# Optimization experiments

Hardware: AMD Instinct MI355X
Metric: run time of the kernel (lower is better)

The kernel has to match this reference:

```python
import jax, jax.numpy as jnp
import numpy as np

K = 5          # number of spline bins
B = 5.0        # tail bound
HIDDEN = 8
MIN_W = 1e-3; MIN_H = 1e-3; MIN_D = 1e-3  # RQS defaults (Durkan et al.)


def setup_inputs() -> dict:
    n, d = 32768, 64
    L = d - 1
    P = 3 * K - 1
    ks = jax.random.split(jax.random.key(0), 8)
    x = jax.random.normal(ks[0], (n, d), jnp.float32) * 2.0
    init_param = jax.random.uniform(ks[1], (P,), jnp.float32, -0.5, 0.5)
    # ragged first layers: layer l (predicts dim l+1) sees x[:, :l+1]; zero-pad to width L
    mask = (jnp.arange(L)[None, :] <= jnp.arange(L)[:, None]).astype(jnp.float32)
    W1 = jax.random.normal(ks[2], (L, L, HIDDEN), jnp.float32) * 0.2 * mask[:, :, None]
    b1 = jax.random.normal(ks[3], (L, HIDDEN), jnp.float32) * 0.1
    W2 = jax.random.normal(ks[4], (L, HIDDEN, HIDDEN), jnp.float32) * 0.2
    b2 = jax.random.normal(ks[5], (L, HIDDEN), jnp.float32) * 0.1
    W3 = jax.random.normal(ks[6], (L, HIDDEN, P), jnp.float32) * 0.2
    b3 = jax.random.normal(ks[7], (L, P), jnp.float32) * 0.1
    return {"x": x, "init_param": init_param, "W1": W1, "b1": b1,
            "W2": W2, "b2": b2, "W3": W3, "b3": b3}


def _rqs(xf, Wu, Hu, Du):
    # xf: (M,), Wu/Hu: (M,K), Du: (M,K-1) -- vectorized unconstrained RQS, forward
    inside = (xf >= -B) & (xf <= B)
    const = float(np.log(np.exp(1.0 - MIN_D) - 1.0))
    Dpad = jnp.pad(Du, ((0, 0), (1, 1)), constant_values=const)

    widths = MIN_W + (1.0 - MIN_W * K) * jax.nn.softmax(Wu, axis=-1)
    cumw = jnp.pad(jnp.cumsum(widths, -1), ((0, 0), (1, 0)))
    cumw = 2.0 * B * cumw - B
    cumw = cumw.at[:, 0].set(-B).at[:, -1].set(B)
    widths = cumw[:, 1:] - cumw[:, :-1]

    heights = MIN_H + (1.0 - MIN_H * K) * jax.nn.softmax(Hu, axis=-1)
    cumh = jnp.pad(jnp.cumsum(heights, -1), ((0, 0), (1, 0)))
    cumh = 2.0 * B * cumh - B
    cumh = cumh.at[:, 0].set(-B).at[:, -1].set(B)
    heights = cumh[:, 1:] - cumh[:, :-1]

    derivs = MIN_D + jax.nn.softplus(Dpad)  # (M, K+1)

    xc = jnp.clip(xf, -B, B)
    idx = jnp.clip(jnp.sum(xc[:, None] >= cumw, axis=-1) - 1, 0, K - 1)
    take = lambda a: jnp.take_along_axis(a, idx[:, None], axis=-1)[:, 0]

    icw, ibw = take(cumw), take(widths)
    ich, ih = take(cumh), take(heights)
    idl = take(heights / widths)
    idv = take(derivs)
    idvp1 = take(derivs[:, 1:])

    theta = (xc - icw) / ibw
    tmt = theta * (1.0 - theta)
    num = ih * (idl * theta * theta + idv * tmt)
    den = idl + (idv + idvp1 - 2.0 * idl) * tmt
    out = ich + num / den
    dnum = idl * idl * (idvp1 * theta * theta + 2.0 * idl * tmt + idv * (1.0 - theta) ** 2)
    ld = jnp.log(dnum) - 2.0 * jnp.log(den)
    return jnp.where(inside, out, xf), jnp.where(inside, ld, 0.0)


def reference(x, init_param, W1, b1, W2, b2, W3, b3):
    n, d = x.shape
    L = d - 1
    P = 3 * K - 1
    # mask re-applied so padded W1 entries are exactly inert (ragged Linear(i, hidden))
    mask = (jnp.arange(L)[None, :] <= jnp.arange(L)[:, None]).astype(x.dtype)
    h = jnp.tanh(jnp.einsum('nj,ljh->lnh', x[:, :L], W1 * mask[:, :, None]) + b1[:, None, :])
    h = jnp.tanh(jnp.einsum('lnh,lhg->lng', h, W2) + b2[:, None, :])
    out = jnp.einsum('lng,lgp->lnp', h, W3) + b3[:, None, :]      # (L, n, P)
    p0 = jnp.broadcast_to(init_param, (1, n, P))                  # dim 0 uses init_param
    params = jnp.concatenate([p0, out], axis=0).reshape(d * n, P)  # dim-major, matches Ws layout
    Wu, Hu, Du = params[:, :K], params[:, K:2 * K], params[:, 2 * K:]
    xf = x.T.reshape(-1)  # x.transpose(0,1).flatten()
    zs, lds = _rqs(xf, Wu, Hu, Du)
    # NOTE: faithfully replicates the original's reshape of the dim-major flat
    # vector directly to (n, d) (as in the torch source).
    return zs.reshape(n, d), lds.reshape(n, d).sum(axis=1)
```

## Files before the change

kernel.cpp:

```cpp
#include <hip/hip_runtime.h>
#include <hip/hip_bf16.h>
#include <math.h>

#define KK 5
#define Bc 5.0f
#define NN 32768
#define DD 64
#define LL 63
#define PP 14
#define MIN_Wc 0.001f
#define MIN_Hc 0.001f
#define MIN_Dc 0.001f

typedef float f4 __attribute__((ext_vector_type(4)));
typedef float f32x4 __attribute__((ext_vector_type(4)));
typedef float f2 __attribute__((ext_vector_type(2)));
typedef short short8 __attribute__((ext_vector_type(8)));

__device__ __forceinline__ float rcp_fast(float v)  { return __builtin_amdgcn_rcpf(v); }
__device__ __forceinline__ float exp_fast(float v)  { return __expf(v); }
__device__ __forceinline__ float log_fast(float v)  { return __logf(v); }
__device__ __forceinline__ float tanh_fast(float v) {
    float e = exp_fast(2.0f * v);
    return 1.0f - 2.0f * rcp_fast(e + 1.0f);
}
__device__ __forceinline__ float softplus_fast(float v) {
    return (v > 15.0f) ? v : log_fast(1.0f + exp_fast(v));
}
__device__ __forceinline__ ushort to_bf16u(float v) {
    __hip_bfloat16 b = __float2bfloat16(v);
    return *(ushort*)&b;
}
__device__ __forceinline__ f2 splat2(float v) { f2 r; r.x = v; r.y = v; return r; }

__global__ __launch_bounds__(256) void pack_b1(const float* __restrict__ W1,
                                               ushort* __restrict__ Bp) {
    int id = blockIdx.x * 256 + threadIdx.x;
    int n = id >> 6, k = id & 63;
    float v = 0.f;
    if (n < 504 && k < 63) {
        int l = n >> 3, h = n & 7;
        v = W1[(l * 63 + k) * 8 + h];
    }
    Bp[id] = to_bf16u(v);
}

__device__ __forceinline__ short8 pack_a(f4 v0, f4 v1) {
    short8 a;
    a[0] = (short)to_bf16u(v0.x); a[1] = (short)to_bf16u(v0.y);
    a[2] = (short)to_bf16u(v0.z); a[3] = (short)to_bf16u(v0.w);
    a[4] = (short)to_bf16u(v1.x); a[5] = (short)to_bf16u(v1.y);
    a[6] = (short)to_bf16u(v1.z); a[7] = (short)to_bf16u(v1.w);
    return a;
}

__device__ __forceinline__ void do_dim(
    int dd, float xf, uint4 hv, int s0, int lane, int bx,
    const float* __restrict__ init_param,
    const float* __restrict__ W2, const float* __restrict__ b2,
    const float* __restrict__ W3, const float* __restrict__ b3,
    float* __restrict__ out)
{
    float p[PP];
    if (dd == 0) {
        #pragma unroll
        for (int i = 0; i < PP; ++i) p[i] = init_param[i];
    } else {
        const int l = dd - 1;
        float h1f[8];
        h1f[0] = __uint_as_float(hv.x << 16);
        h1f[1] = __uint_as_float(hv.x & 0xFFFF0000u);
        h1f[2] = __uint_as_float(hv.y << 16);
        h1f[3] = __uint_as_float(hv.y & 0xFFFF0000u);
        h1f[4] = __uint_as_float(hv.z << 16);
        h1f[5] = __uint_as_float(hv.z & 0xFFFF0000u);
        h1f[6] = __uint_as_float(hv.w << 16);
        h1f[7] = __uint_as_float(hv.w & 0xFFFF0000u);

        const f2* w2p = (const f2*)(W2 + l * 64);
        const f2* b2p = (const f2*)(b2 + l * 8);
        f2 h2p0 = b2p[0], h2p1 = b2p[1], h2p2 = b2p[2], h2p3 = b2p[3];
        #pragma unroll
        for (int h = 0; h < 8; ++h) {
            f2 av = splat2(h1f[h]);
            h2p0 += av * w2p[h * 4];
            h2p1 += av * w2p[h * 4 + 1];
            h2p2 += av * w2p[h * 4 + 2];
            h2p3 += av * w2p[h * 4 + 3];
        }
        float h2f[8];
        h2f[0] = tanh_fast(h2p0.x); h2f[1] = tanh_fast(h2p0.y);
        h2f[2] = tanh_fast(h2p1.x); h2f[3] = tanh_fast(h2p1.y);
        h2f[4] = tanh_fast(h2p2.x); h2f[5] = tanh_fast(h2p2.y);
        h2f[6] = tanh_fast(h2p3.x); h2f[7] = tanh_fast(h2p3.y);

        const f2* w3p = (const f2*)(W3 + l * 112);
        const f2* b3p = (const f2*)(b3 + l * PP);
        f2 pp0 = b3p[0], pp1 = b3p[1], pp2 = b3p[2], pp3 = b3p[3];
        f2 pp4 = b3p[4], pp5 = b3p[5], pp6 = b3p[6];
        #pragma unroll
        for (int g = 0; g < 8; ++g) {
            f2 av = splat2(h2f[g]);
            pp0 += av * w3p[g * 7];
            pp1 += av * w3p[g * 7 + 1];
            pp2 += av * w3p[g * 7 + 2];
            pp3 += av * w3p[g * 7 + 3];
            pp4 += av * w3p[g * 7 + 4];
            pp5 += av * w3p[g * 7 + 5];
            pp6 += av * w3p[g * 7 + 6];
        }
        p[0] = pp0.x; p[1] = pp0.y; p[2]  = pp1.x; p[3]  = pp1.y;
        p[4] = pp2.x; p[5] = pp2.y; p[6]  = pp3.x; p[7]  = pp3.y;
        p[8] = pp4.x; p[9] = pp4.y; p[10] = pp5.x; p[11] = pp5.y;
        p[12] = pp6.x; p[13] = pp6.y;
    }

    f2 e0, e1, e2, e3, e4;
    e0.x = exp_fast(p[0]); e0.y = exp_fast(p[KK]);
    e1.x = exp_fast(p[1]); e1.y = exp_fast(p[KK + 1]);
    e2.x = exp_fast(p[2]); e2.y = exp_fast(p[KK + 2]);
    e3.x = exp_fast(p[3]); e3.y = exp_fast(p[KK + 3]);
    e4.x = exp_fast(p[4]); e4.y = exp_fast(p[KK + 4]);
    f2 es = e0 + e1 + e2 + e3 + e4;
    f2 nrm; nrm.x = 0.995f * rcp_fast(es.x); nrm.y = 0.995f * rcp_fast(es.y);

    const f2 minv = {MIN_Wc, MIN_Hc};
    f2 cb0 = splat2(-Bc), acc2 = splat2(0.f);
    acc2 += minv + nrm * e0;  f2 cb1 = splat2(2.f * Bc) * acc2 - splat2(Bc);
    acc2 += minv + nrm * e1;  f2 cb2 = splat2(2.f * Bc) * acc2 - splat2(Bc);
    acc2 += minv + nrm * e2;  f2 cb3 = splat2(2.f * Bc) * acc2 - splat2(Bc);
    acc2 += minv + nrm * e3;  f2 cb4 = splat2(2.f * Bc) * acc2 - splat2(Bc);
    f2 cb5 = splat2(Bc);

    float d0 = 1.0f, d5 = 1.0f;
    float d1 = MIN_Dc + softplus_fast(p[10]);
    float d2 = MIN_Dc + softplus_fast(p[11]);
    float d3 = MIN_Dc + softplus_fast(p[12]);
    float d4 = MIN_Dc + softplus_fast(p[13]);

    const float xc = fminf(fmaxf(xf, -Bc), Bc);

    float icw = cb0.x, ich = cb0.y;
    float ibw = cb1.x - cb0.x, ih = cb1.y - cb0.y;
    float idv = d0, idvp1 = d1;
    {
        bool c = xc >= cb1.x; f2 dif = cb2 - cb1;
        icw = c ? cb1.x : icw; ich = c ? cb1.y : ich;
        ibw = c ? dif.x : ibw; ih  = c ? dif.y : ih;
        idv = c ? d1 : idv; idvp1 = c ? d2 : idvp1;
    }
    {
        bool c = xc >= cb2.x; f2 dif = cb3 - cb2;
        icw = c ? cb2.x : icw; ich = c ? cb2.y : ich;
        ibw = c ? dif.x : ibw; ih  = c ? dif.y : ih;
        idv = c ? d2 : idv; idvp1 = c ? d3 : idvp1;
    }
    {
        bool c = xc >= cb3.x; f2 dif = cb4 - cb3;
        icw = c ? cb3.x : icw; ich = c ? cb3.y : ich;
        ibw = c ? dif.x : ibw; ih  = c ? dif.y : ih;
        idv = c ? d3 : idv; idvp1 = c ? d4 : idvp1;
    }
    {
        bool c = xc >= cb4.x; f2 dif = cb5 - cb4;
        icw = c ? cb4.x : icw; ich = c ? cb4.y : ich;
        ibw = c ? dif.x : ibw; ih  = c ? dif.y : ih;
        idv = c ? d4 : idv; idvp1 = c ? d5 : idvp1;
    }

    const float ibw_r = rcp_fast(ibw);
    const float idl = ih * ibw_r;
    const float theta = (xc - icw) * ibw_r;
    const float omt = 1.0f - theta;
    const float tmt = theta * omt;
    const float num = ih * (idl * theta * theta + idv * tmt);
    const float den = idl + (idv + idvp1 - 2.0f * idl) * tmt;
    const float dr = rcp_fast(den);
    const float outv = ich + num * dr;
    const float dnum = idl * idl * (idvp1 * theta * theta + 2.0f * idl * tmt + idv * omt * omt);
    const float ld = log_fast(dnum * dr * dr);

    const bool inside = (xf >= -Bc) && (xf <= Bc);
    const float z = inside ? outv : xf;
    float ldv = inside ? ld : 0.0f;

    out[dd * NN + s0 + lane] = z;

    #pragma unroll
    for (int off = 32; off > 0; off >>= 1) ldv += __shfl_down(ldv, off);
    if (lane == 0) out[NN * DD + dd * (NN / 64) + bx] = ldv;
}

#define H1S 136
__global__ __launch_bounds__(256, 8) void fused_kernel(
    const float* __restrict__ x, const float* __restrict__ init_param,
    const ushort* __restrict__ Bp, const float* __restrict__ b1,
    const float* __restrict__ W2, const float* __restrict__ b2,
    const float* __restrict__ W3, const float* __restrict__ b3,
    float* __restrict__ out)
{
    __shared__ ushort h1c[64 * H1S];
    const int tid = threadIdx.x;
    const int s0 = blockIdx.x * 64;
    const int y  = blockIdx.y;
    const int bx = blockIdx.x;
    const int lane = tid & 63;
    const int wave = __builtin_amdgcn_readfirstlane(tid >> 6);
    const int ln = lane & 15, qg = lane >> 4;
    const int m0 = wave * 16;

    const float* xrow = x + (size_t)(s0 + lane) * 64;
    const int db = y * 16 + 1 + wave * 4;
    float xv0 = xrow[db];
    float xv1 = xrow[db + 1];
    float xv2 = xrow[db + 2];
    float xv3 = xrow[(y == 3 && wave == 3) ? 0 : db + 3];

    short8 a0, a1;
    {
        const float* xr = x + (size_t)(s0 + m0 + ln) * 64 + qg * 8;
        a0 = pack_a(*(const f4*)xr, *(const f4*)(xr + 4));
        a1 = (y >= 2) ? pack_a(*(const f4*)(xr + 32), *(const f4*)(xr + 36)) : a0;
    }

    #pragma unroll
    for (int nt = 0; nt < 8; ++nt) {
        int ncol = y * 128 + nt * 16 + ln;
        const short8* bp8 = (const short8*)(Bp + ncol * 64 + qg * 8);
        f32x4 acc = {0.f, 0.f, 0.f, 0.f};
        acc = __builtin_amdgcn_mfma_f32_16x16x32_bf16(a0, bp8[0], acc, 0, 0, 0);
        if (y >= 2)
            acc = __builtin_amdgcn_mfma_f32_16x16x32_bf16(a1, bp8[4], acc, 0, 0, 0);
        float bias = (ncol < 504) ? b1[ncol] : 0.f;
        #pragma unroll
        for (int r = 0; r < 4; ++r) {
            float v = tanh_fast(acc[r] + bias);
            h1c[(m0 + qg * 4 + r) * H1S + nt * 16 + ln] = to_bf16u(v);
        }
    }
    __syncthreads();

    const uint4* hp = (const uint4*)&h1c[lane * H1S + wave * 32];
    uint4 hv0 = hp[0], hv1 = hp[1], hv2 = hp[2], hv3 = hp[3];

    const int d0_ = db;
    do_dim(d0_,     xv0, hv0, s0, lane, bx, init_param, W2, b2, W3, b3, out);
    do_dim(d0_ + 1, xv1, hv1, s0, lane, bx, init_param, W2, b2, W3, b3, out);
    do_dim(d0_ + 2, xv2, hv2, s0, lane, bx, init_param, W2, b2, W3, b3, out);
    do_dim((y == 3 && wave == 3) ? 0 : d0_ + 3,
                    xv3, hv3, s0, lane, bx, init_param, W2, b2, W3, b3, out);
}

extern "C" void kernel_launch(void* const* d_in, const int* in_sizes, int n_in,
                              void* d_out, int out_size, void* d_ws, size_t ws_size,
                              hipStream_t stream) {
    const float* x          = (const float*)d_in[0];
    const float* init_param = (const float*)d_in[1];
    const float* W1         = (const float*)d_in[2];
    const float* b1         = (const float*)d_in[3];
    const float* W2         = (const float*)d_in[4];
    const float* b2         = (const float*)d_in[5];
    const float* W3         = (const float*)d_in[6];
    const float* b3         = (const float*)d_in[7];
    float* out = (float*)d_out;

    ushort* Bp = (ushort*)d_ws;

    pack_b1<<<128, 256, 0, stream>>>(W1, Bp);
    fused_kernel<<<dim3(512, 4), 256, 0, stream>>>(x, init_param, Bp, b1,
                                                   W2, b2, W3, b3, out);
}
```

Measured before the change: 112.3 us.

## Stage per-layer MLP weights in padded LDS and defer softplus to selected bin

Each block now copies the W2, b2, W3 and b3 slices for its 16 layers into shared memory, padded to 16-float rows so the per-lane matvecs use aligned 128-bit LDS reads instead of scalar global loads. The RQS derivative softplus is computed only for the two selected knots instead of all four, which cuts transcendental work. The launch-bounds occupancy hint drops from 8 to 5 to make room for the extra shared memory and registers, so fewer waves may be resident to hide latency.

```diff
diff --git a/kernel.cpp b/kernel.cpp
--- a/kernel.cpp
+++ b/kernel.cpp
@@ -32,6 +32,7 @@
     return *(ushort*)&b;
 }
 __device__ __forceinline__ f2 splat2(float v) { f2 r; r.x = v; r.y = v; return r; }
+__device__ __forceinline__ f4 splat4(float v) { f4 r; r.x = v; r.y = v; r.z = v; r.w = v; return r; }
 
 __global__ __launch_bounds__(256) void pack_b1(const float* __restrict__ W1,
                                                ushort* __restrict__ Bp) {
@@ -54,19 +55,20 @@
     return a;
 }
 
+#define WSL 216
+
 __device__ __forceinline__ void do_dim(
-    int dd, float xf, uint4 hv, int s0, int lane, int bx,
-    const float* __restrict__ init_param,
-    const float* __restrict__ W2, const float* __restrict__ b2,
-    const float* __restrict__ W3, const float* __restrict__ b3,
-    float* __restrict__ out)
+    int dd, const float* wp, float xf, uint4 hv, int s0, int lane, int bx,
+    const float* __restrict__ init_param, float* __restrict__ out)
 {
-    float p[PP];
+    float p0,p1,p2,p3,p4,p5,p6,p7,p8,p9,p10,p11,p12,p13;
     if (dd == 0) {
-        #pragma unroll
-        for (int i = 0; i < PP; ++i) p[i] = init_param[i];
+        p0 = init_param[0];  p1 = init_param[1];  p2 = init_param[2];
+        p3 = init_param[3];  p4 = init_param[4];  p5 = init_param[5];
+        p6 = init_param[6];  p7 = init_param[7];  p8 = init_param[8];
+        p9 = init_param[9];  p10 = init_param[10]; p11 = init_param[11];
+        p12 = init_param[12]; p13 = init_param[13];
     } else {
-        const int l = dd - 1;
         float h1f[8];
         h1f[0] = __uint_as_float(hv.x << 16);
         h1f[1] = __uint_as_float(hv.x & 0xFFFF0000u);
@@ -77,50 +79,51 @@
         h1f[6] = __uint_as_float(hv.w << 16);
         h1f[7] = __uint_as_float(hv.w & 0xFFFF0000u);
 
-        const f2* w2p = (const f2*)(W2 + l * 64);
-        const f2* b2p = (const f2*)(b2 + l * 8);
-        f2 h2p0 = b2p[0], h2p1 = b2p[1], h2p2 = b2p[2], h2p3 = b2p[3];
+        f4 h2a = *(const f4*)(wp + 64);
+        f4 h2b = *(const f4*)(wp + 68);
         #pragma unroll
         for (int h = 0; h < 8; ++h) {
-            f2 av = splat2(h1f[h]);
-            h2p0 += av * w2p[h * 4];
-            h2p1 += av * w2p[h * 4 + 1];
-            h2p2 += av * w2p[h * 4 + 2];
-            h2p3 += av * w2p[h * 4 + 3];
+            f4 wa = *(const f4*)(wp + h * 8);
+            f4 wb = *(const f4*)(wp + h * 8 + 4);
+            f4 av = splat4(h1f[h]);
+            h2a += av * wa;
+            h2b += av * wb;
         }
         float h2f[8];
-        h2f[0] = tanh_fast(h2p0.x); h2f[1] = tanh_fast(h2p0.y);
-        h2f[2] = tanh_fast(h2p1.x); h2f[3] = tanh_fast(h2p1.y);
-        h2f[4] = tanh_fast(h2p2.x); h2f[5] = tanh_fast(h2p2.y);
-        h2f[6] = tanh_fast(h2p3.x); h2f[7] = tanh_fast(h2p3.y);
-
-        const f2* w3p = (const f2*)(W3 + l * 112);
-        const f2* b3p = (const f2*)(b3 + l * PP);
-        f2 pp0 = b3p[0], pp1 = b3p[1], pp2 = b3p[2], pp3 = b3p[3];
-        f2 pp4 = b3p[4], pp5 = b3p[5], pp6 = b3p[6];
+        h2f[0] = tanh_fast(h2a.x); h2f[1] = tanh_fast(h2a.y);
+        h2f[2] = tanh_fast(h2a.z); h2f[3] = tanh_fast(h2a.w);
+        h2f[4] = tanh_fast(h2b.x); h2f[5] = tanh_fast(h2b.y);
+        h2f[6] = tanh_fast(h2b.z); h2f[7] = tanh_fast(h2b.w);
+
+        f4 ppa = *(const f4*)(wp + 200);
+        f4 ppb = *(const f4*)(wp + 204);
+        f4 ppc = *(const f4*)(wp + 208);
+        f4 ppd = *(const f4*)(wp + 212);
         #pragma unroll
         for (int g = 0; g < 8; ++g) {
-            f2 av = splat2(h2f[g]);
-            pp0 += av * w3p[g * 7];
-            pp1 += av * w3p[g * 7 + 1];
-            pp2 += av * w3p[g * 7 + 2];
-            pp3 += av * w3p[g * 7 + 3];
-            pp4 += av * w3p[g * 7 + 4];
-            pp5 += av * w3p[g * 7 + 5];
-            pp6 += av * w3p[g * 7 + 6];
+            const float* wr = wp + 72 + g * 16;
+            f4 w0 = *(const f4*)(wr);
+            f4 w1 = *(const f4*)(wr + 4);
+            f4 w2v = *(const f4*)(wr + 8);
+            f4 w3v = *(const f4*)(wr + 12);
+            f4 av = splat4(h2f[g]);
+            ppa += av * w0;
+            ppb += av * w1;
+            ppc += av * w2v;
+            ppd += av * w3v;
         }
-        p[0] = pp0.x; p[1] = pp0.y; p[2]  = pp1.x; p[3]  = pp1.y;
-        p[4] = pp2.x; p[5] = pp2.y; p[6]  = pp3.x; p[7]  = pp3.y;
-        p[8] = pp4.x; p[9] = pp4.y; p[10] = pp5.x; p[11] = pp5.y;
-        p[12] = pp6.x; p[13] = pp6.y;
+        p0 = ppa.x; p1 = ppa.y; p2 = ppa.z; p3 = ppa.w;
+        p4 = ppb.x; p5 = ppb.y; p6 = ppb.z; p7 = ppb.w;
+        p8 = ppc.x; p9 = ppc.y; p10 = ppc.z; p11 = ppc.w;
+        p12 = ppd.x; p13 = ppd.y;
     }
 
     f2 e0, e1, e2, e3, e4;
-    e0.x = exp_fast(p[0]); e0.y = exp_fast(p[KK]);
-    e1.x = exp_fast(p[1]); e1.y = exp_fast(p[KK + 1]);
-    e2.x = exp_fast(p[2]); e2.y = exp_fast(p[KK + 2]);
-    e3.x = exp_fast(p[3]); e3.y = exp_fast(p[KK + 3]);
-    e4.x = exp_fast(p[4]); e4.y = exp_fast(p[KK + 4]);
+    e0.x = exp_fast(p0); e0.y = exp_fast(p5);
+    e1.x = exp_fast(p1); e1.y = exp_fast(p6);
+    e2.x = exp_fast(p2); e2.y = exp_fast(p7);
+    e3.x = exp_fast(p3); e3.y = exp_fast(p8);
+    e4.x = exp_fast(p4); e4.y = exp_fast(p9);
     f2 es = e0 + e1 + e2 + e3 + e4;
     f2 nrm; nrm.x = 0.995f * rcp_fast(es.x); nrm.y = 0.995f * rcp_fast(es.y);
 
@@ -132,41 +135,38 @@
     acc2 += minv + nrm * e3;  f2 cb4 = splat2(2.f * Bc) * acc2 - splat2(Bc);
     f2 cb5 = splat2(Bc);
 
-    float d0 = 1.0f, d5 = 1.0f;
-    float d1 = MIN_Dc + softplus_fast(p[10]);
-    float d2 = MIN_Dc + softplus_fast(p[11]);
-    float d3 = MIN_Dc + softplus_fast(p[12]);
-    float d4 = MIN_Dc + softplus_fast(p[13]);
-
     const float xc = fminf(fmaxf(xf, -Bc), Bc);
 
     float icw = cb0.x, ich = cb0.y;
     float ibw = cb1.x - cb0.x, ih = cb1.y - cb0.y;
-    float idv = d0, idvp1 = d1;
+    float rv = p10, rvp = p10;
+    bool v_one = true, vp_one = false;
     {
         bool c = xc >= cb1.x; f2 dif = cb2 - cb1;
         icw = c ? cb1.x : icw; ich = c ? cb1.y : ich;
         ibw = c ? dif.x : ibw; ih  = c ? dif.y : ih;
-        idv = c ? d1 : idv; idvp1 = c ? d2 : idvp1;
+        v_one = c ? false : v_one; rv = c ? p10 : rv; rvp = c ? p11 : rvp;
     }
     {
         bool c = xc >= cb2.x; f2 dif = cb3 - cb2;
         icw = c ? cb2.x : icw; ich = c ? cb2.y : ich;
         ibw = c ? dif.x : ibw; ih  = c ? dif.y : ih;
-        idv = c ? d2 : idv; idvp1 = c ? d3 : idvp1;
+        rv = c ? p11 : rv; rvp = c ? p12 : rvp;
     }
     {
         bool c = xc >= cb3.x; f2 dif = cb4 - cb3;
         icw = c ? cb3.x : icw; ich = c ? cb3.y : ich;
         ibw = c ? dif.x : ibw; ih  = c ? dif.y : ih;
-        idv = c ? d3 : idv; idvp1 = c ? d4 : idvp1;
+        rv = c ? p12 : rv; rvp = c ? p13 : rvp;
     }
     {
         bool c = xc >= cb4.x; f2 dif = cb5 - cb4;
         icw = c ? cb4.x : icw; ich = c ? cb4.y : ich;
         ibw = c ? dif.x : ibw; ih  = c ? dif.y : ih;
-        idv = c ? d4 : idv; idvp1 = c ? d5 : idvp1;
-    }
+        rv = c ? p13 : rv; vp_one = c;
+    }
+    const float idv   = v_one  ? 1.0f : MIN_Dc + softplus_fast(rv);
+    const float idvp1 = vp_one ? 1.0f : MIN_Dc + softplus_fast(rvp);
 
     const float ibw_r = rcp_fast(ibw);
     const float idl = ih * ibw_r;
@@ -192,7 +192,7 @@
 }
 
 #define H1S 136
-__global__ __launch_bounds__(256, 8) void fused_kernel(
+__global__ __launch_bounds__(256, 5) void fused_kernel(
     const float* __restrict__ x, const float* __restrict__ init_param,
     const ushort* __restrict__ Bp, const float* __restrict__ b1,
     const float* __restrict__ W2, const float* __restrict__ b2,
@@ -200,6 +200,7 @@
     float* __restrict__ out)
 {
     __shared__ ushort h1c[64 * H1S];
+    __shared__ float  wl[16 * WSL];
     const int tid = threadIdx.x;
     const int s0 = blockIdx.x * 64;
     const int y  = blockIdx.y;
@@ -208,6 +209,7 @@
     const int wave = __builtin_amdgcn_readfirstlane(tid >> 6);
     const int ln = lane & 15, qg = lane >> 4;
     const int m0 = wave * 16;
+    const int l0 = y * 16;
 
     const float* xrow = x + (size_t)(s0 + lane) * 64;
     const int db = y * 16 + 1 + wave * 4;
@@ -221,6 +223,37 @@
         const float* xr = x + (size_t)(s0 + m0 + ln) * 64 + qg * 8;
         a0 = pack_a(*(const f4*)xr, *(const f4*)(xr + 4));
         a1 = (y >= 2) ? pack_a(*(const f4*)(xr + 32), *(const f4*)(xr + 36)) : a0;
+    }
+
+    {
+        int s = tid >> 4, o = (tid & 15) * 4;
+        if (l0 + s < LL)
+            *(f4*)&wl[s * WSL + o] = *(const f4*)&W2[(l0 + s) * 64 + o];
+    }
+    if (tid < 128) {
+        int s = tid >> 3, o = tid & 7;
+        if (l0 + s < LL) wl[s * WSL + 64 + o] = b2[(l0 + s) * 8 + o];
+    }
+    #pragma unroll
+    for (int q0 = 0; q0 < 896; q0 += 256) {
+        int q = q0 + tid;
+        if (q < 896) {
+            int s = q / 56, r = q % 56, g = r / 7, o = r % 7;
+            *(f2*)&wl[s * WSL + 72 + g * 16 + o * 2] =
+                *(const f2*)&W3[(l0 + s) * 112 + g * 14 + o * 2];
+        }
+    }
+    if (tid < 128) {
+        int s = tid >> 3, g = tid & 7;
+        *(f2*)&wl[s * WSL + 72 + g * 16 + 14] = splat2(0.f);
+    }
+    if (tid < 224) {
+        int s = tid / 14, o = tid % 14;
+        wl[s * WSL + 200 + o] = b3[(l0 + s < LL ? l0 + s : 0) * PP + o];
+    }
+    if (tid < 32) {
+        int s = tid >> 1, o = 214 + (tid & 1);
+        wl[s * WSL + o] = 0.f;
     }
 
     #pragma unroll
@@ -243,12 +276,12 @@
     const uint4* hp = (const uint4*)&h1c[lane * H1S + wave * 32];
     uint4 hv0 = hp[0], hv1 = hp[1], hv2 = hp[2], hv3 = hp[3];
 
-    const int d0_ = db;
-    do_dim(d0_,     xv0, hv0, s0, lane, bx, init_param, W2, b2, W3, b3, out);
-    do_dim(d0_ + 1, xv1, hv1, s0, lane, bx, init_param, W2, b2, W3, b3, out);
-    do_dim(d0_ + 2, xv2, hv2, s0, lane, bx, init_param, W2, b2, W3, b3, out);
-    do_dim((y == 3 && wave == 3) ? 0 : d0_ + 3,
-                    xv3, hv3, s0, lane, bx, init_param, W2, b2, W3, b3, out);
+    const int sl = wave * 4;
+    do_dim(db,     wl + (sl)     * WSL, xv0, hv0, s0, lane, bx, init_param, out);
+    do_dim(db + 1, wl + (sl + 1) * WSL, xv1, hv1, s0, lane, bx, init_param, out);
+    do_dim(db + 2, wl + (sl + 2) * WSL, xv2, hv2, s0, lane, bx, init_param, out);
+    do_dim((y == 3 && wave == 3) ? 0 : db + 3,
+                   wl + (sl + 3) * WSL, xv3, hv3, s0, lane, bx, init_param, out);
 }
 
 extern "C" void kernel_launch(void* const* d_in, const int* in_sizes, int n_in,
```

Result: no change. 111.1 us (-1.1%).
